# Kernel tuning notes

Measured on AMD Instinct MI355X. Metric: run time of the kernel, lower is better.

Reference implementation:

```python
import jax, jax.numpy as jnp
import numpy as np
from jax import lax

D, NH, T, DFF, SD = 8, 4, 60, 2048, 17
DH = D // NH
NEG = -1e9

def _ln(x, g, b, eps=1e-5):
    m = jnp.mean(x, -1, keepdims=True)
    v = jnp.mean((x - m) ** 2, -1, keepdims=True)
    return (x - m) / jnp.sqrt(v + eps) * g + b

def _mha(q_in, k_in, v_in, Wqkv, bqkv, Wo, bo, mask):
    Wq, Wk, Wv = jnp.split(Wqkv, 3, axis=0)
    bq, bk, bv = jnp.split(bqkv, 3)
    def proj(x, W, bb):
        B, S, _ = x.shape
        return (x @ W.T + bb).reshape(B, S, NH, DH).transpose(0, 2, 1, 3)
    q = proj(q_in, Wq, bq); k = proj(k_in, Wk, bk); v = proj(v_in, Wv, bv)
    s = jnp.einsum('bhqd,bhkd->bhqk', q, k) / np.float32(np.sqrt(DH))
    s = jnp.where(mask, NEG, s)
    o = jnp.einsum('bhqk,bhkd->bhqd', jax.nn.softmax(s, axis=-1), v)
    B, _, S, _ = o.shape
    return o.transpose(0, 2, 1, 3).reshape(B, S, D) @ Wo.T + bo

def _ffn(x, W1, b1, W2, b2):
    return jax.nn.relu(x @ W1.T + b1) @ W2.T + b2

def _forward(x, emb_W, emb_b, eqW, eqb, eoW, eob, ef1W, ef1b, ef2W, ef2b, el1g, el1b, el2g, el2b, eng, enb, dsqW, dsqb, dsoW, dsob, dcqW, dcqb, dcoW, dcob, df1W, df1b, df2W, df2b, dl1g, dl1b, dl2g, dl2b, dl3g, dl3b, dng, dnb, fc_W, fc_b):
    B = x.shape[0]
    idx = jnp.arange(T)
    causal = (idx[None, :] > idx[:, None])[None, None]  # [1,1,T,T], True = blocked

    @jax.checkpoint
    def step(buf, t):
        keymask = (idx > t)[None, None, None, :]  # positions beyond t are padding
        mem = buf
        for i in range(6):  # nn.Transformer default encoder layers
            mem = _ln(mem + _mha(mem, mem, mem, eqW[i], eqb[i], eoW[i], eob[i], keymask), el1g[i], el1b[i])
            mem = _ln(mem + _ffn(mem, ef1W[i], ef1b[i], ef2W[i], ef2b[i]), el2g[i], el2b[i])
        mem = _ln(mem, eng, enb)
        y = buf
        for i in range(2):  # decoder layers
            y = _ln(y + _mha(y, y, y, dsqW[i], dsqb[i], dsoW[i], dsob[i], causal), dl1g[i], dl1b[i])
            y = _ln(y + _mha(y, mem, mem, dcqW[i], dcqb[i], dcoW[i], dcob[i], keymask), dl2g[i], dl2b[i])
            y = _ln(y + _ffn(y, df1W[i], df1b[i], df2W[i], df2b[i]), dl3g[i], dl3b[i])
        y = _ln(y, dng, dnb)
        st = jnp.take(y, t, axis=1) @ fc_W.T + fc_b  # decoded state at last valid pos [B,17]
        buf = buf.at[:, t + 1].set(st @ emb_W.T + emb_b, mode='drop')
        return buf, st

    buf0 = jnp.zeros((B, T, D), x.dtype).at[:, 0].set(x)
    _, states = lax.scan(step, buf0, idx)
    return jnp.transpose(states, (1, 0, 2))  # [B, T, state_dim]

def setup_inputs() -> dict:
    B = 128
    keys = iter(jax.random.split(jax.random.key(0), 64))
    def W(shape):
        return jax.random.normal(next(keys), shape, jnp.float32) / np.float32(np.sqrt(shape[-1]))
    z = lambda *s: jnp.zeros(s, jnp.float32)
    o = lambda *s: jnp.ones(s, jnp.float32)
    return dict(
        quantized_eos_embedding=jax.random.normal(next(keys), (B, D), jnp.float32),
        emb_W=W((D, SD)), emb_b=z(D),
        eqW=W((6, 3 * D, D)), eqb=z(6, 3 * D), eoW=W((6, D, D)), eob=z(6, D),
        ef1W=W((6, DFF, D)), ef1b=z(6, DFF), ef2W=W((6, D, DFF)), ef2b=z(6, D),
        el1g=o(6, D), el1b=z(6, D), el2g=o(6, D), el2b=z(6, D), eng=o(D), enb=z(D),
        dsqW=W((2, 3 * D, D)), dsqb=z(2, 3 * D), dsoW=W((2, D, D)), dsob=z(2, D),
        dcqW=W((2, 3 * D, D)), dcqb=z(2, 3 * D), dcoW=W((2, D, D)), dcob=z(2, D),
        df1W=W((2, DFF, D)), df1b=z(2, DFF), df2W=W((2, D, DFF)), df2b=z(2, D),
        dl1g=o(2, D), dl1b=z(2, D), dl2g=o(2, D), dl2b=z(2, D), dl3g=o(2, D), dl3b=z(2, D),
        dng=o(D), dnb=z(D),
        fc_W=W((SD, D)), fc_b=z(SD),
    )

def reference(quantized_eos_embedding, emb_W, emb_b, eqW, eqb, eoW, eob, ef1W, ef1b, ef2W, ef2b, el1g, el1b, el2g, el2b, eng, enb, dsqW, dsqb, dsoW, dsob, dcqW, dcqb, dcoW, dcob, df1W, df1b, df2W, df2b, dl1g, dl1b, dl2g, dl2b, dl3g, dl3b, dng, dnb, fc_W, fc_b):
    return _forward(quantized_eos_embedding, emb_W, emb_b, eqW, eqb, eoW, eob, ef1W, ef1b, ef2W, ef2b, el1g, el1b, el2g, el2b, eng, enb, dsqW, dsqb, dsoW, dsob, dcqW, dcqb, dcoW, dcob, df1W, df1b, df2W, df2b, dl1g, dl1b, dl2g, dl2b, dl3g, dl3b, dng, dnb, fc_W, fc_b)
```

## Files before the change

### kernel.cpp

```cpp
#include <hip/hip_runtime.h>


typedef __attribute__((ext_vector_type(8))) short short8;
typedef __attribute__((ext_vector_type(4))) float floatx4;
typedef __attribute__((ext_vector_type(4))) unsigned uint4v;

#define DEV static __device__ __forceinline__

namespace {
constexpr int D   = 8;
constexpr int T   = 60;
constexpr int DFF = 2048;
constexpr int SD  = 17;
constexpr int NT  = 512;
constexpr int NW  = NT / 64;
constexpr int NBLK = DFF / 32;
constexpr int BPW  = NBLK / NW;
constexpr int LSTR = NBLK * 2048;
}

struct Params { const float* in[39]; float* out; };

DEV unsigned short f2bf(float f) {
  unsigned u = __builtin_bit_cast(unsigned, f);
  return (unsigned short)((u + 0x8000u) >> 16);
}
DEV float bf2f(unsigned short h) {
  unsigned u = ((unsigned)h) << 16;
  return __builtin_bit_cast(float, u);
}
DEV floatx4 mfma16(short8 a, short8 b, floatx4 c) {
  return __builtin_amdgcn_mfma_f32_16x16x32_bf16(a, b, c, 0, 0, 0);
}
DEV unsigned cvtpk(float lo, float hi) {
  unsigned r;
  asm("v_cvt_pk_bf16_f32 %0, %1, %2" : "=v"(r) : "v"(lo), "v"(hi));
  return r;
}
DEV float lo2f(unsigned u) { return __builtin_bit_cast(float, u << 16); }
DEV float hi2f(unsigned u) { return __builtin_bit_cast(float, u & 0xffff0000u); }
DEV short8 pack4(unsigned a, unsigned b, unsigned c, unsigned d) {
  uint4v u = {a, b, c, d};
  return __builtin_bit_cast(short8, u);
}

__global__ __launch_bounds__(64) void repack_kernel(Params P, short* ws) {
  const int wg = blockIdx.x;
  const int L = wg >> 6, blk = wg & 63;
  const int l = (int)threadIdx.x, gg = l >> 4, rr = l & 15;
  const float *W1p, *b1p, *W2p;
  if (L < 6) { W1p = P.in[7] + L * 16384;  b1p = P.in[8] + L * 2048;  W2p = P.in[9] + L * 16384; }
  else { int m = L - 6; W1p = P.in[25] + m * 16384; b1p = P.in[26] + m * 2048; W2p = P.in[27] + m * 16384; }
  short* out = ws + (L * 64 + blk) * 2048;
  const int j0 = blk * 32;
  short8 z = {0,0,0,0,0,0,0,0};
  for (int tt = 0; tt < 2; ++tt) {
    int j = j0 + tt * 16 + rr;
    short8 r = z;
    if (gg == 3) {
      unsigned short h = f2bf(b1p[j]);
      r[0] = (short)h; r[1] = (short)f2bf(b1p[j] - bf2f(h));
    } else {
      const float* p = W1p + j * 8;
#pragma unroll
      for (int i = 0; i < 8; ++i) {
        float v = p[i];
        unsigned short h = f2bf(v);
        r[i] = (short)((gg == 1) ? f2bf(v - bf2f(h)) : h);
      }
    }
    *(short8*)(out + tt * 512 + l * 8) = r;
  }
  short8 wh = z, wl = z;
  if (rr < 8) {
#pragma unroll
    for (int i = 0; i < 8; ++i) {
      int j = j0 + (i < 4 ? gg * 4 + i : 16 + gg * 4 + (i - 4));
      float v = W2p[rr * 2048 + j];
      unsigned short h = f2bf(v);
      wh[i] = (short)h;
      wl[i] = (short)f2bf(v - bf2f(h));
    }
  }
  *(short8*)(out + 1024 + l * 8) = wh;
  *(short8*)(out + 1536 + l * 8) = wl;
}

__global__ __launch_bounds__(NT, 2) void tdec_kernel(Params P, const short* ws) {
  const int b    = blockIdx.x;
  const int tid  = (int)threadIdx.x;
  const int lane = tid & 63;
  const int wave = tid >> 6;
  const int gg   = lane >> 4;
  const int rr   = lane & 15;

  __shared__ float buf[T][D];
  __shared__ __align__(16) float X[64][D];
  __shared__ float Mem[64][D];
  __shared__ float Qs[64][D];
  __shared__ float Ks[64][D];
  __shared__ float Vs[64][D];
  __shared__ float ATT[64][D];
  __shared__ __align__(16) float red[NW * 1024];
  __shared__ float wAll[10 * 288];
  __shared__ float lnp[40][D];
  __shared__ float b2all[8][D];
  __shared__ float fcw[SD][D];
  __shared__ float fcbv[SD];
  __shared__ float embw[D][SD];
  __shared__ float embbv[D];
  __shared__ float stv[SD];

  for (int o = tid; o < 2880; o += NT) {
    int a = o / 288, off = o - a * 288;
    const float *Wq, *Bq, *Wo, *Bo; int li;
    if (a < 6)              { li = a;            Wq=P.in[3];  Bq=P.in[4];  Wo=P.in[5];  Bo=P.in[6];  }
    else if (((a - 6) & 1) == 0) { li = (a-6)>>1; Wq=P.in[17]; Bq=P.in[18]; Wo=P.in[19]; Bo=P.in[20]; }
    else                    { li = (a-6)>>1;     Wq=P.in[21]; Bq=P.in[22]; Wo=P.in[23]; Bo=P.in[24]; }
    float v;
    if (off < 192)      v = Wq[li*192 + off];
    else if (off < 216) v = Bq[li*24  + off - 192];
    else if (off < 280) v = Wo[li*64  + off - 216];
    else                v = Bo[li*8   + off - 280];
    wAll[o] = v;
  }
  for (int o = tid; o < 320; o += NT) {
    int row = o >> 3, k = o & 7;
    const float* src;
    if (row < 24) { int li = row >> 2, w = row & 3;
      src = (w==0 ? P.in[11] : w==1 ? P.in[12] : w==2 ? P.in[13] : P.in[14]) + li*8;
    } else if (row < 26) src = (row == 24 ? P.in[15] : P.in[16]);
    else if (row < 38) { int q = row - 26, li = q / 6, w = q - li*6;
      src = (w==0?P.in[29]:w==1?P.in[30]:w==2?P.in[31]:w==3?P.in[32]:w==4?P.in[33]:P.in[34]) + li*8;
    } else src = (row == 38 ? P.in[35] : P.in[36]);
    lnp[row][k] = src[k];
  }
  if (tid < 64) { int row = tid >> 3, k = tid & 7;
    b2all[row][k] = (row < 6) ? P.in[10][row*8 + k] : P.in[28][(row-6)*8 + k]; }
  if (tid < 136) fcw[tid >> 3][tid & 7] = P.in[37][tid];
  if (tid < SD)  fcbv[tid] = P.in[38][tid];
  if (tid < 136) embw[tid / 17][tid % 17] = P.in[1][tid];
  if (tid < D)   embbv[tid] = P.in[2][tid];
  if (tid < D)   buf[0][tid] = P.in[0][b*D + tid];
  __syncthreads();

  const short8 zero8 = {0,0,0,0,0,0,0,0};
  const floatx4 zf4  = {0.f,0.f,0.f,0.f};

  auto proj8 = [&](float (*dst)[D], const float (*src)[D], const float* w,
                   const float* bias, int R) {
    for (int o = tid; o < (R << 3); o += NT) {
      int r = o >> 3, d = o & 7;
      const float* wr = w + d * 8;
      const float* xr = src[r];
      float s = bias[d];
#pragma unroll
      for (int k = 0; k < 8; ++k) s += xr[k] * wr[k];
      dst[r][d] = s;
    }
  };

  auto attn = [&](int R, bool causal) {
    if (R <= 32) {
      int p = tid >> 4, h2 = ((tid >> 2) & 3) << 1, e = tid & 3;
      if (p < R) {
        float q0 = Qs[p][h2]     * 0.70710678118654752f;
        float q1 = Qs[p][h2 + 1] * 0.70710678118654752f;
        int lim = causal ? p : (R - 1);
        float l = 0.f, a0 = 0.f, a1 = 0.f;
        for (int j = e; j <= lim; j += 4) {
          float s = q0 * Ks[j][h2] + q1 * Ks[j][h2 + 1] - 10.f;
          float ev = __expf(s);
          l += ev; a0 += ev * Vs[j][h2]; a1 += ev * Vs[j][h2 + 1];
        }
        l  += __shfl_xor(l, 1);  l  += __shfl_xor(l, 2);
        a0 += __shfl_xor(a0, 1); a0 += __shfl_xor(a0, 2);
        a1 += __shfl_xor(a1, 1); a1 += __shfl_xor(a1, 2);
        if (e == 0) {
          float rl = 1.f / l;
          ATT[p][h2] = a0 * rl; ATT[p][h2 + 1] = a1 * rl;
        }
      }
    } else {
      int p = tid >> 3, h2 = ((tid >> 1) & 3) << 1, e = tid & 1;
      if (p < R) {
        float q0 = Qs[p][h2]     * 0.70710678118654752f;
        float q1 = Qs[p][h2 + 1] * 0.70710678118654752f;
        int lim = causal ? p : (R - 1);
        float l = 0.f, a0 = 0.f, a1 = 0.f;
        for (int j = e; j <= lim; j += 2) {
          float s = q0 * Ks[j][h2] + q1 * Ks[j][h2 + 1] - 10.f;
          float ev = __expf(s);
          l += ev; a0 += ev * Vs[j][h2]; a1 += ev * Vs[j][h2 + 1];
        }
        l  += __shfl_xor(l, 1);
        a0 += __shfl_xor(a0, 1);
        a1 += __shfl_xor(a1, 1);
        if (e == 0) {
          float rl = 1.f / l;
          ATT[p][h2] = a0 * rl; ATT[p][h2 + 1] = a1 * rl;
        }
      }
    }
  };

  auto oproj_ln = [&](const float* wo, const float* bo, const float* g,
                      const float* bb, int R) {
    if (tid < R) {
      float o[8];
#pragma unroll
      for (int d = 0; d < 8; ++d) {
        float s = bo[d] + X[tid][d];
#pragma unroll
        for (int k = 0; k < 8; ++k) s += ATT[tid][k] * wo[d * 8 + k];
        o[d] = s;
      }
      float m = 0.f;
#pragma unroll
      for (int k = 0; k < 8; ++k) m += o[k];
      m *= 0.125f;
      float v = 0.f;
#pragma unroll
      for (int k = 0; k < 8; ++k) { float dm = o[k] - m; v += dm * dm; }
      float rs = rsqrtf(v * 0.125f + 1e-5f);
#pragma unroll
      for (int k = 0; k < 8; ++k) X[tid][k] = (o[k] - m) * rs * g[k] + bb[k];
    }
  };

  auto ln_rows = [&](float (*dst)[D], const float (*src)[D], const float* g,
                     const float* bb, int R) {
    if (tid < R) {
      float o[8];
#pragma unroll
      for (int k = 0; k < 8; ++k) o[k] = src[tid][k];
      float m = 0.f;
#pragma unroll
      for (int k = 0; k < 8; ++k) m += o[k];
      m *= 0.125f;
      float v = 0.f;
#pragma unroll
      for (int k = 0; k < 8; ++k) { float dm = o[k] - m; v += dm * dm; }
      float rs = rsqrtf(v * 0.125f + 1e-5f);
#pragma unroll
      for (int k = 0; k < 8; ++k) dst[tid][k] = (o[k] - m) * rs * g[k] + bb[k];
    }
  };

  auto mha = [&](int a, float (*kvsrc)[D], bool causal, int R,
                 const float* g, const float* bb) {
    const float* wq = &wAll[a * 288];
    proj8(Qs, X,     wq +   0, wq + 192, R);
    proj8(Ks, kvsrc, wq +  64, wq + 200, R);
    proj8(Vs, kvsrc, wq + 128, wq + 208, R);
    __syncthreads();
    attn(R, causal);
    __syncthreads();
    oproj_ln(wq + 216, wq + 280, g, bb, R);
    __syncthreads();
  };

  auto mha_row = [&](int a, float (*kvsrc)[D], int R, int t,
                     const float* g, const float* bb) {
    const float* wq = &wAll[a * 288];
    proj8(Ks, kvsrc, wq +  64, wq + 200, R);
    proj8(Vs, kvsrc, wq + 128, wq + 208, R);
    if (tid < 8) {
      int d = tid;
      const float* wr = wq + d * 8;
      float s = wq[192 + d];
#pragma unroll
      for (int k = 0; k < 8; ++k) s += X[t][k] * wr[k];
      Qs[t][d] = s;
    }
    __syncthreads();
    if (tid < 32) {
      int h2 = (tid >> 3) << 1, e = tid & 7;
      float q0 = Qs[t][h2]     * 0.70710678118654752f;
      float q1 = Qs[t][h2 + 1] * 0.70710678118654752f;
      float l = 0.f, a0 = 0.f, a1 = 0.f;
      for (int j = e; j < R; j += 8) {
        float s = q0 * Ks[j][h2] + q1 * Ks[j][h2 + 1] - 10.f;
        float ev = __expf(s);
        l += ev; a0 += ev * Vs[j][h2]; a1 += ev * Vs[j][h2 + 1];
      }
      l  += __shfl_xor(l, 1);  l  += __shfl_xor(l, 2);  l  += __shfl_xor(l, 4);
      a0 += __shfl_xor(a0, 1); a0 += __shfl_xor(a0, 2); a0 += __shfl_xor(a0, 4);
      a1 += __shfl_xor(a1, 1); a1 += __shfl_xor(a1, 2); a1 += __shfl_xor(a1, 4);
      if (e == 0) {
        float rl = 1.f / l;
        ATT[t][h2] = a0 * rl; ATT[t][h2 + 1] = a1 * rl;
      }
    }
    __syncthreads();
    if (tid == 0) {
      float o[8];
#pragma unroll
      for (int d = 0; d < 8; ++d) {
        float s = wq[280 + d] + X[t][d];
#pragma unroll
        for (int k = 0; k < 8; ++k) s += ATT[t][k] * wq[216 + d * 8 + k];
        o[d] = s;
      }
      float m = 0.f;
#pragma unroll
      for (int k = 0; k < 8; ++k) m += o[k];
      m *= 0.125f;
      float v = 0.f;
#pragma unroll
      for (int k = 0; k < 8; ++k) { float dm = o[k] - m; v += dm * dm; }
      float rs = rsqrtf(v * 0.125f + 1e-5f);
#pragma unroll
      for (int k = 0; k < 8; ++k) X[t][k] = (o[k] - m) * rs * g[k] + bb[k];
    }
    __syncthreads();
  };

  auto ffn = [&](const short* wsL, const float* b2, const float* g,
                 const float* bb, int R, int Mt) {
    const short* pb = wsL + (wave * BPW) * 2048;
    short8 a0  = *(const short8*)(pb + lane * 8);
    short8 a1  = *(const short8*)(pb + 512 + lane * 8);
    short8 w2h = *(const short8*)(pb + 1024 + lane * 8);
    short8 w2l = *(const short8*)(pb + 1536 + lane * 8);

    short8 bx[4];
#pragma unroll
    for (int mt = 0; mt < 4; ++mt) {
      short8 v = zero8;
      if (mt < Mt) {
        if (gg == 3) { v[0] = (short)0x3F80; v[1] = (short)0x3F80; }
        else {
          int r = mt * 16 + rr;
          float4 A = *(const float4*)&X[r][0];
          float4 Bv = *(const float4*)&X[r][4];
          unsigned u0 = cvtpk(A.x, A.y), u1 = cvtpk(A.z, A.w);
          unsigned u2 = cvtpk(Bv.x, Bv.y), u3 = cvtpk(Bv.z, Bv.w);
          if (gg == 2) {
            unsigned l0 = cvtpk(A.x - lo2f(u0), A.y - hi2f(u0));
            unsigned l1 = cvtpk(A.z - lo2f(u1), A.w - hi2f(u1));
            unsigned l2 = cvtpk(Bv.x - lo2f(u2), Bv.y - hi2f(u2));
            unsigned l3 = cvtpk(Bv.z - lo2f(u3), Bv.w - hi2f(u3));
            v = pack4(l0, l1, l2, l3);
          } else {
            v = pack4(u0, u1, u2, u3);
          }
        }
      }
      bx[mt] = v;
    }

    floatx4 acc[4] = {zf4, zf4, zf4, zf4};
    for (int blkI = 0; blkI < BPW; ++blkI) {
      short8 na0 = zero8, na1 = zero8, nw2h = zero8, nw2l = zero8;
      if (blkI + 1 < BPW) {
        const short* pn = pb + (blkI + 1) * 2048;
        na0  = *(const short8*)(pn + lane * 8);
        na1  = *(const short8*)(pn + 512 + lane * 8);
        nw2h = *(const short8*)(pn + 1024 + lane * 8);
        nw2l = *(const short8*)(pn + 1536 + lane * 8);
      }
#pragma unroll
      for (int mt = 0; mt < 4; ++mt) {
        if (mt < Mt) {
          floatx4 h0 = mfma16(a0, bx[mt], zf4);
          floatx4 h1 = mfma16(a1, bx[mt], zf4);
          float v0 = fmaxf(h0[0], 0.f), v1 = fmaxf(h0[1], 0.f);
          float v2 = fmaxf(h0[2], 0.f), v3 = fmaxf(h0[3], 0.f);
          float v4 = fmaxf(h1[0], 0.f), v5 = fmaxf(h1[1], 0.f);
          float v6 = fmaxf(h1[2], 0.f), v7 = fmaxf(h1[3], 0.f);
          unsigned u0 = cvtpk(v0, v1), u1 = cvtpk(v2, v3);
          unsigned u2 = cvtpk(v4, v5), u3 = cvtpk(v6, v7);
          unsigned l0 = cvtpk(v0 - lo2f(u0), v1 - hi2f(u0));
          unsigned l1 = cvtpk(v2 - lo2f(u1), v3 - hi2f(u1));
          unsigned l2 = cvtpk(v4 - lo2f(u2), v5 - hi2f(u2));
          unsigned l3 = cvtpk(v6 - lo2f(u3), v7 - hi2f(u3));
          short8 ah = pack4(u0, u1, u2, u3);
          short8 al = pack4(l0, l1, l2, l3);
          acc[mt] = mfma16(w2h, ah, acc[mt]);
          acc[mt] = mfma16(w2h, al, acc[mt]);
          acc[mt] = mfma16(w2l, ah, acc[mt]);
        }
      }
      a0 = na0; a1 = na1; w2h = nw2h; w2l = nw2l;
    }

#pragma unroll
    for (int mt = 0; mt < 4; ++mt)
      if (mt < Mt)
        *(floatx4*)&red[(((wave << 2) + mt) << 8) + (lane << 2)] = acc[mt];
    __syncthreads();
    if (tid < R) {
      int r = tid, mt = r >> 4, rl = r & 15;
      float o[8];
#pragma unroll
      for (int d = 0; d < 8; ++d) {
        float s = X[r][d] + b2[d];
        int base = (mt << 8) + ((((d >> 2) << 4) + rl) << 2) + (d & 3);
#pragma unroll
        for (int w = 0; w < NW; ++w) s += red[(w << 10) + base];
        o[d] = s;
      }
      float m = 0.f;
#pragma unroll
      for (int k = 0; k < 8; ++k) m += o[k];
      m *= 0.125f;
      float var = 0.f;
#pragma unroll
      for (int k = 0; k < 8; ++k) { float dm = o[k] - m; var += dm * dm; }
      float rs = rsqrtf(var * 0.125f + 1e-5f);
#pragma unroll
      for (int k = 0; k < 8; ++k) X[r][k] = (o[k] - m) * rs * g[k] + bb[k];
    }
    __syncthreads();
  };

  auto ffn_row = [&](const short* wsL, const float* b2, const float* g,
                     const float* bb, int t) {
    const short* pb = wsL + (wave * BPW) * 2048;
    short8 a0  = *(const short8*)(pb + lane * 8);
    short8 a1  = *(const short8*)(pb + 512 + lane * 8);
    short8 w2h = *(const short8*)(pb + 1024 + lane * 8);
    short8 w2l = *(const short8*)(pb + 1536 + lane * 8);

    short8 bx = zero8;
    if (gg == 3) { bx[0] = (short)0x3F80; bx[1] = (short)0x3F80; }
    else if (rr == 0) {
      float4 A = *(const float4*)&X[t][0];
      float4 Bv = *(const float4*)&X[t][4];
      unsigned u0 = cvtpk(A.x, A.y), u1 = cvtpk(A.z, A.w);
      unsigned u2 = cvtpk(Bv.x, Bv.y), u3 = cvtpk(Bv.z, Bv.w);
      if (gg == 2) {
        unsigned l0 = cvtpk(A.x - lo2f(u0), A.y - hi2f(u0));
        unsigned l1 = cvtpk(A.z - lo2f(u1), A.w - hi2f(u1));
        unsigned l2 = cvtpk(Bv.x - lo2f(u2), Bv.y - hi2f(u2));
        unsigned l3 = cvtpk(Bv.z - lo2f(u3), Bv.w - hi2f(u3));
        bx = pack4(l0, l1, l2, l3);
      } else {
        bx = pack4(u0, u1, u2, u3);
      }
    }

    floatx4 acc = zf4;
    for (int blkI = 0; blkI < BPW; ++blkI) {
      short8 na0 = zero8, na1 = zero8, nw2h = zero8, nw2l = zero8;
      if (blkI + 1 < BPW) {
        const short* pn = pb + (blkI + 1) * 2048;
        na0  = *(const short8*)(pn + lane * 8);
        na1  = *(const short8*)(pn + 512 + lane * 8);
        nw2h = *(const short8*)(pn + 1024 + lane * 8);
        nw2l = *(const short8*)(pn + 1536 + lane * 8);
      }
      floatx4 h0 = mfma16(a0, bx, zf4);
      floatx4 h1 = mfma16(a1, bx, zf4);
      float v0 = fmaxf(h0[0], 0.f), v1 = fmaxf(h0[1], 0.f);
      float v2 = fmaxf(h0[2], 0.f), v3 = fmaxf(h0[3], 0.f);
      float v4 = fmaxf(h1[0], 0.f), v5 = fmaxf(h1[1], 0.f);
      float v6 = fmaxf(h1[2], 0.f), v7 = fmaxf(h1[3], 0.f);
      unsigned u0 = cvtpk(v0, v1), u1 = cvtpk(v2, v3);
      unsigned u2 = cvtpk(v4, v5), u3 = cvtpk(v6, v7);
      unsigned l0 = cvtpk(v0 - lo2f(u0), v1 - hi2f(u0));
      unsigned l1 = cvtpk(v2 - lo2f(u1), v3 - hi2f(u1));
      unsigned l2 = cvtpk(v4 - lo2f(u2), v5 - hi2f(u2));
      unsigned l3 = cvtpk(v6 - lo2f(u3), v7 - hi2f(u3));
      short8 ah = pack4(u0, u1, u2, u3);
      short8 al = pack4(l0, l1, l2, l3);
      acc = mfma16(w2h, ah, acc);
      acc = mfma16(w2h, al, acc);
      acc = mfma16(w2l, ah, acc);
      a0 = na0; a1 = na1; w2h = nw2h; w2l = nw2l;
    }

    *(floatx4*)&red[(wave << 10) + (lane << 2)] = acc;
    __syncthreads();
    if (tid == 0) {
      float o[8];
#pragma unroll
      for (int d = 0; d < 8; ++d) {
        float s = X[t][d] + b2[d];
        int base = ((d >> 2) << 6) + (d & 3);
#pragma unroll
        for (int w = 0; w < NW; ++w) s += red[(w << 10) + base];
        o[d] = s;
      }
      float m = 0.f;
#pragma unroll
      for (int k = 0; k < 8; ++k) m += o[k];
      m *= 0.125f;
      float var = 0.f;
#pragma unroll
      for (int k = 0; k < 8; ++k) { float dm = o[k] - m; var += dm * dm; }
      float rs = rsqrtf(var * 0.125f + 1e-5f);
#pragma unroll
      for (int k = 0; k < 8; ++k) X[t][k] = (o[k] - m) * rs * g[k] + bb[k];
    }
    __syncthreads();
  };

  for (int t = 0; t < T; ++t) {
    const int R = t + 1;
    const int Mt = (R + 15) >> 4;

    for (int o = tid; o < 512; o += NT) {
      int r = o >> 3, d = o & 7;
      X[r][d] = (r < R) ? buf[r][d] : 0.f;
    }
    __syncthreads();

    for (int li = 0; li < 6; ++li) {
      mha(li, X, false, R, lnp[li * 4 + 0], lnp[li * 4 + 1]);
      ffn(ws + li * LSTR, b2all[li], lnp[li * 4 + 2], lnp[li * 4 + 3], R, Mt);
    }
    ln_rows(X, X, lnp[24], lnp[25], R);
    __syncthreads();
    for (int o = tid; o < 512; o += NT) {
      int r = o >> 3, d = o & 7;
      if (r < R) Mem[r][d] = X[r][d];
      X[r][d] = (r < R) ? buf[r][d] : 0.f;
    }
    __syncthreads();

    mha(6, X,   true,  R, lnp[26], lnp[27]);
    mha(7, Mem, false, R, lnp[28], lnp[29]);
    ffn(ws + 6 * LSTR, b2all[6], lnp[30], lnp[31], R, Mt);

    mha_row(8, X,   R, t, lnp[32], lnp[33]);
    mha_row(9, Mem, R, t, lnp[34], lnp[35]);
    ffn_row(ws + 7 * LSTR, b2all[7], lnp[36], lnp[37], t);

    if (tid == 0) {
      float o[8];
#pragma unroll
      for (int k = 0; k < 8; ++k) o[k] = X[t][k];
      float m = 0.f;
#pragma unroll
      for (int k = 0; k < 8; ++k) m += o[k];
      m *= 0.125f;
      float v = 0.f;
#pragma unroll
      for (int k = 0; k < 8; ++k) { float dm = o[k] - m; v += dm * dm; }
      float rs = rsqrtf(v * 0.125f + 1e-5f);
#pragma unroll
      for (int k = 0; k < 8; ++k) X[t][k] = (o[k] - m) * rs * lnp[38][k] + lnp[39][k];
    }
    __syncthreads();
    if (tid < SD) {
      float s = fcbv[tid];
#pragma unroll
      for (int k = 0; k < 8; ++k) s += X[t][k] * fcw[tid][k];
      stv[tid] = s;
      P.out[(b * T + t) * SD + tid] = s;
    }
    __syncthreads();
    if (t + 1 < T && tid < D) {
      float s = embbv[tid];
#pragma unroll
      for (int k = 0; k < SD; ++k) s += stv[k] * embw[tid][k];
      buf[t + 1][tid] = s;
    }
    __syncthreads();
  }
}

extern "C" void kernel_launch(void* const* d_in, const int* in_sizes, int n_in,
                              void* d_out, int out_size, void* d_ws, size_t ws_size,
                              hipStream_t stream) {
  (void)in_sizes; (void)n_in; (void)ws_size; (void)out_size;
  Params P;
  for (int i = 0; i < 39; ++i) P.in[i] = (const float*)d_in[i];
  P.out = (float*)d_out;
  short* ws = (short*)d_ws;
  repack_kernel<<<dim3(8 * NBLK), dim3(64), 0, stream>>>(P, ws);
  tdec_kernel<<<dim3(128), dim3(NT), 0, stream>>>(P, ws);
}
```

Baseline: 3.473 ms.

## Double block size to 1024 threads and fold extra waves into reduction

Raises the workgroup from 512 to 1024 threads so the FFN blocks are split across 16 waves instead of 8. The shared reduction buffer is kept at 8 slots: the upper 8 waves add their partials into the lower waves' slots after an extra barrier. Attention thread mapping is widened to use more lanes per query row. The intent is more parallelism per sequence to cut latency of the serial per-step work. The cost is an extra __syncthreads per FFN, more register pressure without the 2-blocks occupancy hint, and heavier barriers.

Result: slower. 3.776 ms (+8.7%).

```diff
diff --git a/kernel.cpp b/kernel.cpp
--- a/kernel.cpp
+++ b/kernel.cpp
@@ -12,8 +12,9 @@
 constexpr int T   = 60;
 constexpr int DFF = 2048;
 constexpr int SD  = 17;
-constexpr int NT  = 512;
+constexpr int NT  = 1024;
 constexpr int NW  = NT / 64;
+constexpr int NRED = 8;
 constexpr int NBLK = DFF / 32;
 constexpr int BPW  = NBLK / NW;
 constexpr int LSTR = NBLK * 2048;
@@ -86,7 +87,7 @@
   *(short8*)(out + 1536 + l * 8) = wl;
 }
 
-__global__ __launch_bounds__(NT, 2) void tdec_kernel(Params P, const short* ws) {
+__global__ __launch_bounds__(NT) void tdec_kernel(Params P, const short* ws) {
   const int b    = blockIdx.x;
   const int tid  = (int)threadIdx.x;
   const int lane = tid & 63;
@@ -101,7 +102,7 @@
   __shared__ float Ks[64][D];
   __shared__ float Vs[64][D];
   __shared__ float ATT[64][D];
-  __shared__ __align__(16) float red[NW * 1024];
+  __shared__ __align__(16) float red[NRED * 1024];
   __shared__ float wAll[10 * 288];
   __shared__ float lnp[40][D];
   __shared__ float b2all[8][D];
@@ -162,6 +163,26 @@
 
   auto attn = [&](int R, bool causal) {
     if (R <= 32) {
+      int p = tid >> 5, h2 = ((tid >> 3) & 3) << 1, e = tid & 7;
+      if (p < R) {
+        float q0 = Qs[p][h2]     * 0.70710678118654752f;
+        float q1 = Qs[p][h2 + 1] * 0.70710678118654752f;
+        int lim = causal ? p : (R - 1);
+        float l = 0.f, a0 = 0.f, a1 = 0.f;
+        for (int j = e; j <= lim; j += 8) {
+          float s = q0 * Ks[j][h2] + q1 * Ks[j][h2 + 1] - 10.f;
+          float ev = __expf(s);
+          l += ev; a0 += ev * Vs[j][h2]; a1 += ev * Vs[j][h2 + 1];
+        }
+        l  += __shfl_xor(l, 1);  l  += __shfl_xor(l, 2);  l  += __shfl_xor(l, 4);
+        a0 += __shfl_xor(a0, 1); a0 += __shfl_xor(a0, 2); a0 += __shfl_xor(a0, 4);
+        a1 += __shfl_xor(a1, 1); a1 += __shfl_xor(a1, 2); a1 += __shfl_xor(a1, 4);
+        if (e == 0) {
+          float rl = 1.f / l;
+          ATT[p][h2] = a0 * rl; ATT[p][h2 + 1] = a1 * rl;
+        }
+      }
+    } else {
       int p = tid >> 4, h2 = ((tid >> 2) & 3) << 1, e = tid & 3;
       if (p < R) {
         float q0 = Qs[p][h2]     * 0.70710678118654752f;
@@ -176,26 +197,6 @@
         l  += __shfl_xor(l, 1);  l  += __shfl_xor(l, 2);
         a0 += __shfl_xor(a0, 1); a0 += __shfl_xor(a0, 2);
         a1 += __shfl_xor(a1, 1); a1 += __shfl_xor(a1, 2);
-        if (e == 0) {
-          float rl = 1.f / l;
-          ATT[p][h2] = a0 * rl; ATT[p][h2 + 1] = a1 * rl;
-        }
-      }
-    } else {
-      int p = tid >> 3, h2 = ((tid >> 1) & 3) << 1, e = tid & 1;
-      if (p < R) {
-        float q0 = Qs[p][h2]     * 0.70710678118654752f;
-        float q1 = Qs[p][h2 + 1] * 0.70710678118654752f;
-        int lim = causal ? p : (R - 1);
-        float l = 0.f, a0 = 0.f, a1 = 0.f;
-        for (int j = e; j <= lim; j += 2) {
-          float s = q0 * Ks[j][h2] + q1 * Ks[j][h2 + 1] - 10.f;
-          float ev = __expf(s);
-          l += ev; a0 += ev * Vs[j][h2]; a1 += ev * Vs[j][h2 + 1];
-        }
-        l  += __shfl_xor(l, 1);
-        a0 += __shfl_xor(a0, 1);
-        a1 += __shfl_xor(a1, 1);
         if (e == 0) {
           float rl = 1.f / l;
           ATT[p][h2] = a0 * rl; ATT[p][h2 + 1] = a1 * rl;
@@ -385,10 +386,22 @@
       a0 = na0; a1 = na1; w2h = nw2h; w2l = nw2l;
     }
 
-#pragma unroll
-    for (int mt = 0; mt < 4; ++mt)
-      if (mt < Mt)
-        *(floatx4*)&red[(((wave << 2) + mt) << 8) + (lane << 2)] = acc[mt];
+    if (wave < 8) {
+#pragma unroll
+      for (int mt = 0; mt < 4; ++mt)
+        if (mt < Mt)
+          *(floatx4*)&red[(((wave << 2) + mt) << 8) + (lane << 2)] = acc[mt];
+    }
+    __syncthreads();
+    if (wave >= 8) {
+#pragma unroll
+      for (int mt = 0; mt < 4; ++mt)
+        if (mt < Mt) {
+          float* p = &red[((((wave - 8) << 2) + mt) << 8) + (lane << 2)];
+          floatx4 cur = *(floatx4*)p;
+          *(floatx4*)p = cur + acc[mt];
+        }
+    }
     __syncthreads();
     if (tid < R) {
       int r = tid, mt = r >> 4, rl = r & 15;
@@ -398,7 +411,7 @@
         float s = X[r][d] + b2[d];
         int base = (mt << 8) + ((((d >> 2) << 4) + rl) << 2) + (d & 3);
 #pragma unroll
-        for (int w = 0; w < NW; ++w) s += red[(w << 10) + base];
+        for (int w = 0; w < NRED; ++w) s += red[(w << 10) + base];
         o[d] = s;
       }
       float m = 0.f;
@@ -471,7 +484,14 @@
       a0 = na0; a1 = na1; w2h = nw2h; w2l = nw2l;
     }
 
-    *(floatx4*)&red[(wave << 10) + (lane << 2)] = acc;
+    if (wave < 8)
+      *(floatx4*)&red[(wave << 10) + (lane << 2)] = acc;
+    __syncthreads();
+    if (wave >= 8) {
+      float* p = &red[((wave - 8) << 10) + (lane << 2)];
+      floatx4 cur = *(floatx4*)p;
+      *(floatx4*)p = cur + acc;
+    }
     __syncthreads();
     if (tid == 0) {
       float o[8];
@@ -480,7 +500,7 @@
         float s = X[t][d] + b2[d];
         int base = ((d >> 2) << 6) + (d & 3);
 #pragma unroll
-        for (int w = 0; w < NW; ++w) s += red[(w << 10) + base];
+        for (int w = 0; w < NRED; ++w) s += red[(w << 10) + base];
         o[d] = s;
       }
       float m = 0.f;
```
